# Performance work log

Hardware: AMD Instinct MI355X
Metric: run time of the kernel (lower is better)

Reference implementation:

```python
import jax, jax.numpy as jnp
import numpy as np
import math

DIM = 768
HEADS = 12
HEAD_DIM = DIM // HEADS
LENS_T = 64
LENS_S = 256
NTOK = LENS_T + LENS_S
BATCH = 32
MLP_HIDDEN = 4 * DIM
KEEP_RATIO = 0.7
LENS_KEEP = math.ceil(KEEP_RATIO * LENS_S)  # 180, static
NEG_INF = -1e9  # finite stand-in for masked_fill(-inf); mask is all-False here
LN_EPS = 1e-5


def layer_norm(x, g, b):
    m = jnp.mean(x, axis=-1, keepdims=True)
    v = jnp.var(x, axis=-1, keepdims=True)
    return (x - m) * jax.lax.rsqrt(v + LN_EPS) * g + b


def attention(x_normed, w_qkv, w_proj, b_proj, mask):
    # x_normed: [B,N,C]; torch: qkv Linear (no bias), split heads, softmax(qk*scale), proj
    B, N, C = x_normed.shape
    qkv = (x_normed @ w_qkv.T).reshape(B, N, 3, HEADS, HEAD_DIM)
    qkv = jnp.transpose(qkv, (2, 0, 3, 1, 4))  # [3,B,H,N,Dh]
    q, k, v = qkv[0], qkv[1], qkv[2]
    scores = jnp.einsum('bhqd,bhkd->bhqk', q, k) * (HEAD_DIM ** -0.5)
    scores = jnp.where(mask[:, None, None, :], NEG_INF, scores)
    attn = jax.nn.softmax(scores, axis=-1)  # [B,H,N,N]
    out = jnp.einsum('bhqk,bhkd->bhqd', attn, v)
    out = jnp.transpose(out, (0, 2, 1, 3)).reshape(B, N, C)
    return out @ w_proj.T + b_proj, attn


def mlp(x, w_fc1, b_fc1, w_fc2, b_fc2):
    h = jax.nn.gelu(x @ w_fc1.T + b_fc1, approximate=False)
    return h @ w_fc2.T + b_fc2


def candidate_topk(attn_all, tmpl_mask_f):
    # attn_all: [B,H,N,N]; template->search block, masked mean over template rows,
    # mean over heads, sort descending, split into keep/removed.
    attn_ts = attn_all[:, :, :LENS_T, LENS_T:]  # [B,H,T,S]
    w = tmpl_mask_f[:, None, :, None]  # [B,1,T,1]
    denom = jnp.sum(tmpl_mask_f, axis=1)[:, None, None]  # [B,1,1]
    scores = jnp.sum(attn_ts * w, axis=2) / denom  # [B,H,S] mean over kept template rows
    scores = jnp.mean(scores, axis=1)  # [B,S] mean over heads
    order = jnp.argsort(-scores, axis=1)  # descending
    return order[:, :LENS_KEEP], order[:, LENS_KEEP:]


def gather_tokens(tokens, topk_idx):
    tokens_t = tokens[:, :LENS_T]
    tokens_s = tokens[:, LENS_T:]
    kept = jnp.take_along_axis(tokens_s, topk_idx[:, :, None], axis=1)
    return jnp.concatenate([tokens_t, kept], axis=1)


def setup_inputs() -> dict:
    key = jax.random.key(0)
    ks = jax.random.split(key, 12)
    s = 0.02
    return {
        'x_rgb': jax.random.normal(ks[0], (BATCH, NTOK, DIM), jnp.float32),
        'x_tir': jax.random.normal(ks[1], (BATCH, NTOK, DIM), jnp.float32),
        'global_index_t': jax.random.randint(ks[2], (BATCH, LENS_T), 0, 64).astype(jnp.int64),
        'global_index_s': jax.random.randint(ks[3], (BATCH, LENS_S), 0, 256).astype(jnp.int64),
        'mask': jnp.zeros((BATCH, NTOK), dtype=bool),
        'cte_template_mask': jnp.ones((BATCH, LENS_T), dtype=bool),
        'keep_ratio_search': 0,
        'js_loss': jax.random.normal(ks[4], (1,), jnp.float32),
        'g1': jnp.ones((DIM,), jnp.float32),
        'b1': jnp.zeros((DIM,), jnp.float32),
        'w_qkv': jax.random.normal(ks[5], (3 * DIM, DIM), jnp.float32) * s,
        'w_proj': jax.random.normal(ks[6], (DIM, DIM), jnp.float32) * s,
        'b_proj': jnp.zeros((DIM,), jnp.float32),
        'g2': jnp.ones((DIM,), jnp.float32),
        'b2': jnp.zeros((DIM,), jnp.float32),
        'w_fc1': jax.random.normal(ks[7], (MLP_HIDDEN, DIM), jnp.float32) * s,
        'b_fc1': jnp.zeros((MLP_HIDDEN,), jnp.float32),
        'w_fc2': jax.random.normal(ks[8], (DIM, MLP_HIDDEN), jnp.float32) * s,
        'b_fc2': jnp.zeros((DIM,), jnp.float32),
    }


def reference(x_rgb, x_tir, global_index_t, global_index_s, mask, cte_template_mask,
              keep_ratio_search, js_loss, g1, b1, w_qkv, w_proj, b_proj, g2, b2,
              w_fc1, b_fc1, w_fc2, b_fc2):
    # dual-stream shared-weight attention
    rgb_attn_out, corrmap_rgb = attention(layer_norm(x_rgb, g1, b1), w_qkv, w_proj, b_proj, mask)
    tir_attn_out, corrmap_tir = attention(layer_norm(x_tir, g1, b1), w_qkv, w_proj, b_proj, mask)
    x_rgb = x_rgb + rgb_attn_out  # drop_path = Identity
    x_tir = x_tir + tir_attn_out

    # candidate elimination: both streams use the SAME fused attention map,
    # so the topk is identical for rgb and tir (torch calls it twice, same result)
    attn_all = corrmap_rgb + corrmap_tir
    tmpl_mask_f = cte_template_mask.astype(attn_all.dtype)
    topk_idx, non_topk_idx = candidate_topk(attn_all, tmpl_mask_f)
    x_rgb = gather_tokens(x_rgb, topk_idx)
    x_tir = gather_tokens(x_tir, topk_idx)
    global_index_s_new = jnp.take_along_axis(global_index_s, topk_idx, axis=1)
    removed_index_s = jnp.take_along_axis(global_index_s, non_topk_idx, axis=1)

    x_rgb = x_rgb + mlp(layer_norm(x_rgb, g2, b2), w_fc1, b_fc1, w_fc2, b_fc2)
    x_tir = x_tir + mlp(layer_norm(x_tir, g2, b2), w_fc1, b_fc1, w_fc2, b_fc2)
    return (x_rgb, x_tir, global_index_t, global_index_s_new, removed_index_s,
            corrmap_rgb, corrmap_tir, js_loss)
```

## Files before the change

### kernel.cpp

```cpp
#include <hip/hip_runtime.h>

typedef long long LL;
typedef unsigned short ushort_t;
typedef __attribute__((ext_vector_type(8))) short bfrag;
typedef __attribute__((ext_vector_type(8))) _Float16 hfrag;
typedef __attribute__((ext_vector_type(4))) float facc;
typedef __attribute__((ext_vector_type(4))) unsigned short us4;

constexpr int CDIM  = 768;
constexpr int HEADS = 12;
constexpr int LT    = 64;
constexpr int NTOK  = 320;
constexpr int BATCH = 32;
constexpr int LKEEP = 180;
constexpr int LREM  = 76;
constexpr int NK    = 244;

constexpr LL O_XRGB = 0;
constexpr LL O_XTIR = 5996544;
constexpr LL O_GIT  = 11993088;
constexpr LL O_GSN  = 11995136;
constexpr LL O_REM  = 12000896;
constexpr LL O_CR   = 12003328;
constexpr LL O_CT   = 51324928;
constexpr LL O_JS   = 90646528;

constexpr LL W_X1   = 0;
constexpr LL W_X1G  = 15728640;
constexpr LL W_XN   = 27746304;
constexpr LL W_QKV  = 35610624;
constexpr LL W_ATT  = 59596800;

constexpr LL SZH = 7864320;

__device__ inline ushort_t cvt_bf16(float f) {
    union { float f; unsigned u; } x; x.f = f;
    unsigned u = x.u + 0x7fffu + ((x.u >> 16) & 1u);
    return (ushort_t)(u >> 16);
}
union h16u { _Float16 h; ushort_t u; };

#define GLL(gp, lp) __builtin_amdgcn_global_load_lds( \
    (const __attribute__((address_space(1))) unsigned int*)(gp), \
    (__attribute__((address_space(3))) unsigned int*)(lp), 16, 0, 0)

__device__ inline void xcd_decode(int& bx, int& by) {
    int gx = gridDim.x;
    int nwg = gx * gridDim.y;
    int bid = blockIdx.y * gx + blockIdx.x;
    int q = nwg >> 3, r = nwg & 7;
    int xcd = bid & 7, i = bid >> 3;
    int wg = (xcd < r ? xcd * (q + 1) : r * (q + 1) + (xcd - r) * q) + i;
    bx = wg % gx;
    by = wg / gx;
}

__global__ __launch_bounds__(256)
void prep_weights(const float* __restrict__ wproj, const float* __restrict__ wqkv,
                  const float* __restrict__ wfc1, const float* __restrict__ wfc2,
                  ushort_t* __restrict__ WPROJb, ushort_t* __restrict__ Wh,
                  ushort_t* __restrict__ Wl, ushort_t* __restrict__ WFC1b,
                  ushort_t* __restrict__ WFC2b)
{
    int i = blockIdx.x * 256 + threadIdx.x;
    if (i < 147456) {
        int j = i * 4;
        float4 v = *(const float4*)(wproj + j);
        us4 o;
        o[0] = cvt_bf16(v.x); o[1] = cvt_bf16(v.y);
        o[2] = cvt_bf16(v.z); o[3] = cvt_bf16(v.w);
        *(us4*)(WPROJb + j) = o;
    } else if (i < 589824) {
        int j = (i - 147456) * 4;
        float4 v = *(const float4*)(wqkv + j);
        us4 h, l;
        #pragma unroll
        for (int k = 0; k < 4; ++k) {
            float f = (k == 0 ? v.x : k == 1 ? v.y : k == 2 ? v.z : v.w);
            h16u hh, ll;
            hh.h = (_Float16)f;
            ll.h = (_Float16)(f - (float)hh.h);
            h[k] = hh.u; l[k] = ll.u;
        }
        *(us4*)(Wh + j) = h;
        *(us4*)(Wl + j) = l;
    } else if (i < 1179648) {
        int j = (i - 589824) * 4;
        float4 v = *(const float4*)(wfc1 + j);
        us4 o;
        o[0] = cvt_bf16(v.x); o[1] = cvt_bf16(v.y);
        o[2] = cvt_bf16(v.z); o[3] = cvt_bf16(v.w);
        *(us4*)(WFC1b + j) = o;
    } else {
        int j = (i - 1179648) * 4;
        float4 v = *(const float4*)(wfc2 + j);
        us4 o;
        o[0] = cvt_bf16(v.x); o[1] = cvt_bf16(v.y);
        o[2] = cvt_bf16(v.z); o[3] = cvt_bf16(v.w);
        *(us4*)(WFC2b + j) = o;
    }
}

template<bool B16OUT>
__global__ __launch_bounds__(256)
void ln_kernel(const float* __restrict__ x, const float* __restrict__ g,
               const float* __restrict__ bta, void* __restrict__ y)
{
    LL row = blockIdx.x;
    const float* xr = x + row * 768;
    int t = threadIdx.x;
    float v0 = xr[t], v1 = xr[t + 256], v2 = xr[t + 512];
    __shared__ float red[256];
    red[t] = v0 + v1 + v2;
    __syncthreads();
    for (int s = 128; s; s >>= 1) { if (t < s) red[t] += red[t + s]; __syncthreads(); }
    float mean = red[0] / 768.0f;
    __syncthreads();
    float d0 = v0 - mean, d1 = v1 - mean, d2 = v2 - mean;
    red[t] = d0 * d0 + d1 * d1 + d2 * d2;
    __syncthreads();
    for (int s = 128; s; s >>= 1) { if (t < s) red[t] += red[t + s]; __syncthreads(); }
    float var = red[0] / 768.0f;
    float rs = 1.0f / sqrtf(var + 1e-5f);
    float o0 = d0 * rs * g[t]       + bta[t];
    float o1 = d1 * rs * g[t + 256] + bta[t + 256];
    float o2 = d2 * rs * g[t + 512] + bta[t + 512];
    if (B16OUT) {
        ushort_t* yr = (ushort_t*)y + row * 768;
        yr[t] = cvt_bf16(o0); yr[t + 256] = cvt_bf16(o1); yr[t + 512] = cvt_bf16(o2);
    } else {
        float* yr = (float*)y + row * 768;
        yr[t] = o0; yr[t + 256] = o1; yr[t + 512] = o2;
    }
}

__global__ __launch_bounds__(256)
void ln_f16x2(const float* __restrict__ x0, const float* __restrict__ x1,
              const float* __restrict__ g, const float* __restrict__ bta,
              ushort_t* __restrict__ ybase)
{
    int row = blockIdx.x;
    int mod = row >= 10240;
    int lrow = row - mod * 10240;
    const float* xr = (mod ? x1 : x0) + (LL)lrow * 768;
    ushort_t* yh = ybase + (LL)mod * 2 * SZH + (LL)lrow * 768;
    ushort_t* yl = yh + SZH;
    int t = threadIdx.x;
    float v0 = xr[t], v1 = xr[t + 256], v2 = xr[t + 512];
    __shared__ float red[256];
    red[t] = v0 + v1 + v2;
    __syncthreads();
    for (int s = 128; s; s >>= 1) { if (t < s) red[t] += red[t + s]; __syncthreads(); }
    float mean = red[0] / 768.0f;
    __syncthreads();
    float d0 = v0 - mean, d1 = v1 - mean, d2 = v2 - mean;
    red[t] = d0 * d0 + d1 * d1 + d2 * d2;
    __syncthreads();
    for (int s = 128; s; s >>= 1) { if (t < s) red[t] += red[t + s]; __syncthreads(); }
    float var = red[0] / 768.0f;
    float rs = 1.0f / sqrtf(var + 1e-5f);
    #pragma unroll
    for (int c = 0; c < 3; ++c) {
        float d = (c == 0 ? d0 : c == 1 ? d1 : d2);
        int idx = t + c * 256;
        float o = d * rs * g[idx] + bta[idx];
        h16u hi, lo;
        hi.h = (_Float16)o;
        lo.h = (_Float16)(o - (float)hi.h);
        yh[idx] = hi.u;
        yl[idx] = lo.u;
    }
}

__global__ __launch_bounds__(256)
void gemm_qkv(const ushort_t* __restrict__ Ah, const ushort_t* __restrict__ Al,
              const ushort_t* __restrict__ Bh, const ushort_t* __restrict__ Bl,
              ushort_t* __restrict__ Q1, ushort_t* __restrict__ Q2,
              ushort_t* __restrict__ K1, ushort_t* __restrict__ K2,
              ushort_t* __restrict__ Vt)
{
    __shared__ ushort_t Ahs[8192], Als[8192], Bhs[8192], Bls[8192];
    int bx, by;
    xcd_decode(bx, by);
    const int t = threadIdx.x;
    const int wave = t >> 6, lane = t & 63;
    const int wr = wave >> 1, wc = wave & 1;
    const int lr = lane & 15, lh = lane >> 4;
    const LL bm = (LL)by * 128, bn = (LL)bx * 128;
    const bool vt = (bx >= 12);

    facc acc[4][4];
    #pragma unroll
    for (int i = 0; i < 4; ++i)
        #pragma unroll
        for (int j = 0; j < 4; ++j) acc[i][j] = (facc)(0.0f);

    const LL soff = (bm + wave * 16 + (lane >> 2)) * (LL)768 + (lane & 3) * 8;
    const LL boff = (bn + wave * 16 + (lane >> 2)) * (LL)768 + (lane & 3) * 8;
    const LL a64 = (LL)64 * 768;

    GLL(Ah + soff,       &Ahs[wave * 512]);
    GLL(Ah + soff + a64, &Ahs[2048 + wave * 512]);
    GLL(Bh + boff,       &Bhs[wave * 512]);
    GLL(Bh + boff + a64, &Bhs[2048 + wave * 512]);
    if (!vt) {
        GLL(Al + soff,       &Als[wave * 512]);
        GLL(Al + soff + a64, &Als[2048 + wave * 512]);
        GLL(Bl + boff,       &Bls[wave * 512]);
        GLL(Bl + boff + a64, &Bls[2048 + wave * 512]);
    }
    __syncthreads();

    int cur = 0;
    for (int k0 = 0; k0 < 768; k0 += 32) {
        int nb = (cur ^ 1) * 4096;
        if (k0 + 32 < 768) {
            GLL(Ah + soff + k0 + 32,       &Ahs[nb + wave * 512]);
            GLL(Ah + soff + k0 + 32 + a64, &Ahs[nb + 2048 + wave * 512]);
            GLL(Bh + boff + k0 + 32,       &Bhs[nb + wave * 512]);
            GLL(Bh + boff + k0 + 32 + a64, &Bhs[nb + 2048 + wave * 512]);
            if (!vt) {
                GLL(Al + soff + k0 + 32,       &Als[nb + wave * 512]);
                GLL(Al + soff + k0 + 32 + a64, &Als[nb + 2048 + wave * 512]);
                GLL(Bl + boff + k0 + 32,       &Bls[nb + wave * 512]);
                GLL(Bl + boff + k0 + 32 + a64, &Bls[nb + 2048 + wave * 512]);
            }
        }
        int cb = cur * 4096;
        hfrag ah[4], bh[4];
        #pragma unroll
        for (int mi = 0; mi < 4; ++mi)
            ah[mi] = *(const hfrag*)&Ahs[cb + (wr * 64 + mi * 16 + lr) * 32 + lh * 8];
        #pragma unroll
        for (int ni = 0; ni < 4; ++ni)
            bh[ni] = *(const hfrag*)&Bhs[cb + (wc * 64 + ni * 16 + lr) * 32 + lh * 8];
        if (!vt) {
            hfrag al[4], bl[4];
            #pragma unroll
            for (int mi = 0; mi < 4; ++mi)
                al[mi] = *(const hfrag*)&Als[cb + (wr * 64 + mi * 16 + lr) * 32 + lh * 8];
            #pragma unroll
            for (int ni = 0; ni < 4; ++ni)
                bl[ni] = *(const hfrag*)&Bls[cb + (wc * 64 + ni * 16 + lr) * 32 + lh * 8];
            #pragma unroll
            for (int mi = 0; mi < 4; ++mi)
                #pragma unroll
                for (int ni = 0; ni < 4; ++ni) {
                    acc[mi][ni] = __builtin_amdgcn_mfma_f32_16x16x32_f16(al[mi], bh[ni], acc[mi][ni], 0, 0, 0);
                    acc[mi][ni] = __builtin_amdgcn_mfma_f32_16x16x32_f16(ah[mi], bl[ni], acc[mi][ni], 0, 0, 0);
                    acc[mi][ni] = __builtin_amdgcn_mfma_f32_16x16x32_f16(ah[mi], bh[ni], acc[mi][ni], 0, 0, 0);
                }
        } else {
            #pragma unroll
            for (int mi = 0; mi < 4; ++mi)
                #pragma unroll
                for (int ni = 0; ni < 4; ++ni)
                    acc[mi][ni] = __builtin_amdgcn_mfma_f32_16x16x32_f16(ah[mi], bh[ni], acc[mi][ni], 0, 0, 0);
        }
        __syncthreads();
        cur ^= 1;
    }

    #pragma unroll
    for (int mi = 0; mi < 4; ++mi)
        #pragma unroll
        for (int ni = 0; ni < 4; ++ni)
            #pragma unroll
            for (int j = 0; j < 4; ++j) {
                int r = (int)bm + wr * 64 + mi * 16 + lh * 4 + j;
                int c = (int)bn + wc * 64 + ni * 16 + lr;
                int b = r / 320, tt = r - b * 320;
                int s = c / 768, rem = c - s * 768;
                int h = rem >> 6, d = rem & 63;
                LL hb = (LL)(b * 12 + h) * 20480;
                float v = acc[mi][ni][j];
                if (s == 2) {
                    Vt[hb + d * 320 + tt] = cvt_bf16(v);
                } else {
                    h16u a1, a2;
                    a1.h = (_Float16)v;
                    a2.h = (_Float16)(v - (float)a1.h);
                    LL idx = hb + (LL)tt * 64 + d;
                    if (s == 0) { Q1[idx] = a1.u; Q2[idx] = a2.u; }
                    else        { K1[idx] = a1.u; K2[idx] = a2.u; }
                }
            }
}

__global__ __launch_bounds__(256, 2)
void fused_attn(const ushort_t* __restrict__ Qh, const ushort_t* __restrict__ Qm,
                const ushort_t* __restrict__ Kh, const ushort_t* __restrict__ Km,
                const ushort_t* __restrict__ Vt,
                float* __restrict__ corr, ushort_t* __restrict__ attb,
                double* __restrict__ part, int mod)
{
    __shared__ __align__(128) unsigned char lds[81920];
    constexpr int PS = 40960;

    const int t = threadIdx.x;
    const int wave = t >> 6, lane = t & 63;
    const int lr = lane & 15, lh = lane >> 4;
    const int id  = blockIdx.x;
    const int xcd = id & 7;
    const int rem = id >> 3;
    const int grp = rem / 5;
    const int r0i = rem - grp * 5;
    const int bh  = grp * 8 + xcd;
    const int b = bh / 12, h = bh - b * 12;
    const int r0 = r0i * 64;
    const LL kvbase = (LL)bh * 20480;

    const LL qoff = kvbase + (LL)(r0 + wave * 16 + lr) * 64 + lh * 8;
    hfrag qh0 = *(const hfrag*)(Qh + qoff), qh1 = *(const hfrag*)(Qh + qoff + 32);
    hfrag qm0 = *(const hfrag*)(Qm + qoff), qm1 = *(const hfrag*)(Qm + qoff + 32);

    facc sacc[20];
    #pragma unroll
    for (int ct = 0; ct < 20; ++ct) sacc[ct] = (facc)(0.0f);

    #pragma unroll
    for (int ha = 0; ha < 5; ++ha) {
        if (ha) __syncthreads();
        #pragma unroll
        for (int i = 0; i < 4; ++i) {
            int id2 = wave * 4 + i;
            int s = id2 >> 3, c = id2 & 7;
            int local = c * 1024 + lane * 16;
            int row = local >> 7;
            int sb = local ^ ((row & 7) << 4);
            LL src = kvbase + (LL)ha * 4096 + (sb >> 1);
            const ushort_t* kp = (s == 0) ? Kh : Km;
            GLL(kp + src, &lds[s * 8192 + c * 1024]);
        }
        __syncthreads();

        #pragma unroll
        for (int ctl = 0; ctl < 4; ++ctl) {
            int tokl = ctl * 16 + lr;
            int x = (tokl & 7) << 4;
            const unsigned char* kb = lds + tokl * 128;
            int o0 = (lh * 16) ^ x;
            int o1 = (64 + lh * 16) ^ x;
            hfrag kh0 = *(const hfrag*)(kb + o0);
            hfrag kh1 = *(const hfrag*)(kb + o1);
            hfrag km0 = *(const hfrag*)(kb + 8192 + o0);
            hfrag km1 = *(const hfrag*)(kb + 8192 + o1);
            facc a = sacc[ha * 4 + ctl];
            a = __builtin_amdgcn_mfma_f32_16x16x32_f16(qm0, kh0, a, 0, 0, 0);
            a = __builtin_amdgcn_mfma_f32_16x16x32_f16(qh0, km0, a, 0, 0, 0);
            a = __builtin_amdgcn_mfma_f32_16x16x32_f16(qh0, kh0, a, 0, 0, 0);
            a = __builtin_amdgcn_mfma_f32_16x16x32_f16(qm1, kh1, a, 0, 0, 0);
            a = __builtin_amdgcn_mfma_f32_16x16x32_f16(qh1, km1, a, 0, 0, 0);
            a = __builtin_amdgcn_mfma_f32_16x16x32_f16(qh1, kh1, a, 0, 0, 0);
            sacc[ha * 4 + ctl] = a;
        }
    }

    __syncthreads();

    #pragma unroll
    for (int i = 0; i < 10; ++i) {
        int chunk = wave * 10 + i;
        int gs = chunk * 1024 + lane * 16;
        int d = gs / 640;
        int w = gs - d * 640;
        int sb = d * 640 + (w ^ ((d & 7) << 4));
        GLL(Vt + kvbase + (sb >> 1), &lds[chunk * 1024]);
    }

    float rs4[4];
    #pragma unroll
    for (int j = 0; j < 4; ++j) {
        float m = sacc[0][j];
        #pragma unroll
        for (int ct = 1; ct < 20; ++ct) m = fmaxf(m, sacc[ct][j]);
        #pragma unroll
        for (int o = 1; o < 16; o <<= 1) m = fmaxf(m, __shfl_xor(m, o, 64));
        m *= 0.125f;
        float s = 0.0f;
        #pragma unroll
        for (int ct = 0; ct < 20; ++ct) {
            float e = expf(sacc[ct][j] * 0.125f - m);
            sacc[ct][j] = e;
            s += e;
        }
        #pragma unroll
        for (int o = 1; o < 16; o <<= 1) s += __shfl_xor(s, o, 64);
        float rs = 1.0f / s;
        rs4[j] = rs;

        int prow = wave * 16 + lh * 4 + j;
        int xr = (prow & 7) << 4;
        #pragma unroll
        for (int ct = 0; ct < 20; ++ct) {
            int pcol = ct * 16 + lr;
            *(ushort_t*)(lds + PS + prow * 640 + ((pcol * 2) ^ xr)) =
                cvt_bf16(sacc[ct][j] * rs);
        }
    }

    __syncthreads();

    facc oacc[4];
    #pragma unroll
    for (int dt = 0; dt < 4; ++dt) oacc[dt] = (facc)(0.0f);
    int prow2 = wave * 16 + lr;
    int xp = (prow2 & 7) << 4;
    #pragma unroll
    for (int k0 = 0; k0 < 10; ++k0) {
        bfrag pa = *(const bfrag*)(lds + PS + prow2 * 640 + ((k0 * 64 + lh * 16) ^ xp));
        #pragma unroll
        for (int dt = 0; dt < 4; ++dt) {
            int dcol = dt * 16 + lr;
            bfrag vb = *(const bfrag*)(lds + dcol * 640 + ((k0 * 64 + lh * 16) ^ ((dcol & 7) << 4)));
            oacc[dt] = __builtin_amdgcn_mfma_f32_16x16x32_bf16(pa, vb, oacc[dt], 0, 0, 0);
        }
    }
    #pragma unroll
    for (int dt = 0; dt < 4; ++dt)
        #pragma unroll
        for (int j = 0; j < 4; ++j) {
            int grow = r0 + wave * 16 + lh * 4 + j;
            int gcol = h * 64 + dt * 16 + lr;
            attb[(LL)(b * 320 + grow) * 768 + gcol] = cvt_bf16(oacc[dt][j]);
        }

    __syncthreads();

    #pragma unroll
    for (int ct = 0; ct < 20; ++ct) {
        int pcol = ct * 16 + lr;
        #pragma unroll
        for (int j = 0; j < 4; ++j) {
            int prow = wave * 16 + lh * 4 + j;
            *(float*)(lds + (prow * 320 + pcol) * 4) = sacc[ct][j] * rs4[j];
        }
    }
    __syncthreads();

    float* crow = corr + (LL)bh * 102400 + (LL)r0 * 320;
    #pragma unroll
    for (int i = 0; i < 20; ++i) {
        int idx = i * 256 + t;
        int row = idx / 80, c4 = idx - row * 80;
        float4 v = *(const float4*)(lds + (row * 320 + c4 * 4) * 4);
        *(float4*)(crow + row * 320 + c4 * 4) = v;
    }

    if (r0i == 0) {
        double s64 = 0.0;
        for (int r = 0; r < 64; ++r)
            s64 += (double)*(const float*)(lds + (r * 320 + 64 + t) * 4);
        part[((LL)mod * 384 + bh) * 256 + t] = s64;
    }
}

template<int EPI>
__global__ __launch_bounds__(256)
void gemm_mfma(const ushort_t* __restrict__ A, const ushort_t* __restrict__ B,
               void* __restrict__ Cv, const float* __restrict__ bias,
               const float* __restrict__ res, const int* __restrict__ amap,
               int K, int lda, int ldb, int ldc, int ldres)
{
    __shared__ ushort_t As[8192];
    __shared__ ushort_t Bs[8192];
    int bx, by;
    xcd_decode(bx, by);
    const int t = threadIdx.x;
    const int wave = t >> 6, lane = t & 63;
    const int wr = wave >> 1, wc = wave & 1;
    const LL bm = (LL)by * 128, bn = (LL)bx * 128;

    facc acc[4][4];
    #pragma unroll
    for (int i = 0; i < 4; ++i)
        #pragma unroll
        for (int j = 0; j < 4; ++j) acc[i][j] = (facc)(0.0f);

    const int lr = lane & 15, lh = lane >> 4;
    int r1 = (int)bm + wave * 16 + (lane >> 2);
    int r2 = r1 + 64;
    if (amap) { r1 = amap[r1]; r2 = amap[r2]; }
    const ushort_t* gA1 = A + (LL)r1 * lda + (lane & 3) * 8;
    const ushort_t* gA2 = A + (LL)r2 * lda + (lane & 3) * 8;
    const ushort_t* gB = B + (bn + wave * 16 + (lane >> 2)) * ldb + (lane & 3) * 8;
    const LL b64 = (LL)64 * ldb;

    GLL(gA1,       &As[wave * 512]);
    GLL(gA2,       &As[2048 + wave * 512]);
    GLL(gB,        &Bs[wave * 512]);
    GLL(gB + b64,  &Bs[2048 + wave * 512]);
    __syncthreads();

    int cur = 0;
    for (int k0 = 0; k0 < K; k0 += 32) {
        int nb = (cur ^ 1) * 4096;
        if (k0 + 32 < K) {
            GLL(gA1 + k0 + 32,       &As[nb + wave * 512]);
            GLL(gA2 + k0 + 32,       &As[nb + 2048 + wave * 512]);
            GLL(gB + k0 + 32,        &Bs[nb + wave * 512]);
            GLL(gB + k0 + 32 + b64,  &Bs[nb + 2048 + wave * 512]);
        }
        int cb = cur * 4096;
        bfrag a[4], b[4];
        #pragma unroll
        for (int m = 0; m < 4; ++m)
            a[m] = *(const bfrag*)&As[cb + (wr * 64 + m * 16 + lr) * 32 + lh * 8];
        #pragma unroll
        for (int n = 0; n < 4; ++n)
            b[n] = *(const bfrag*)&Bs[cb + (wc * 64 + n * 16 + lr) * 32 + lh * 8];
        #pragma unroll
        for (int m = 0; m < 4; ++m)
            #pragma unroll
            for (int n = 0; n < 4; ++n)
                acc[m][n] = __builtin_amdgcn_mfma_f32_16x16x32_bf16(a[m], b[n], acc[m][n], 0, 0, 0);
        __syncthreads();
        cur ^= 1;
    }

    #pragma unroll
    for (int m = 0; m < 4; ++m) {
        #pragma unroll
        for (int n = 0; n < 4; ++n) {
            #pragma unroll
            for (int j = 0; j < 4; ++j) {
                LL r = bm + wr * 64 + m * 16 + lh * 4 + j;
                LL c = bn + wc * 64 + n * 16 + lr;
                float v = acc[m][n][j] + bias[c];
                if (EPI == 1) {
                    v = 0.5f * v * (erff(v * 0.70710678118654752f) + 1.0f);
                    ((ushort_t*)Cv)[r * ldc + c] = cvt_bf16(v);
                } else {
                    LL rr = amap ? (LL)amap[r] : r;
                    v += res[rr * ldres + c];
                    ((float*)Cv)[r * ldc + c] = v;
                }
            }
        }
    }
}

__global__ __launch_bounds__(256)
void rank_all(const double* __restrict__ part, const int* __restrict__ gis,
              const int* __restrict__ git, const float* __restrict__ js,
              int* __restrict__ srcmap, float* __restrict__ out)
{
    int b = blockIdx.x, j = threadIdx.x;
    double acc = 0.0;
    for (int h = 0; h < 12; ++h) {
        LL i0 = ((LL)(b * 12 + h)) * 256 + j;
        acc += (part[i0] + part[98304 + i0]) / 64.0;
    }
    double sj = acc / 12.0;
    __shared__ double s[256];
    __shared__ int sord[256];
    s[j] = sj;
    __syncthreads();
    int r = 0;
    for (int i = 0; i < 256; ++i) {
        double si = s[i];
        r += (si > sj) || (si == sj && i < j);
    }
    sord[r] = j;
    float gv = (float)gis[b * 256 + j];
    if (r < LKEEP) out[O_GSN + b * LKEEP + r] = gv;
    else           out[O_REM + b * LREM + (r - LKEEP)] = gv;
    __syncthreads();
    if (j < NK) {
        int src = (j < LT) ? j : (LT + sord[j - LT]);
        srcmap[b * NK + j] = b * NTOK + src;
    }
    if (j < 64) out[O_GIT + b * 64 + j] = (float)git[b * 64 + j];
    if (b == 0 && j == 0) out[O_JS] = js[0];
}

extern "C" void kernel_launch(void* const* d_in, const int* in_sizes, int n_in,
                              void* d_out, int out_size, void* d_ws, size_t ws_size,
                              hipStream_t stream)
{
    const float* xin_m[2] = { (const float*)d_in[0], (const float*)d_in[1] };
    const int*   git    = (const int*)d_in[2];
    const int*   gis    = (const int*)d_in[3];
    const float* js     = (const float*)d_in[7];
    const float* g1     = (const float*)d_in[8];
    const float* b1     = (const float*)d_in[9];
    const float* w_qkv  = (const float*)d_in[10];
    const float* w_proj = (const float*)d_in[11];
    const float* b_proj = (const float*)d_in[12];
    const float* g2     = (const float*)d_in[13];
    const float* b2     = (const float*)d_in[14];
    const float* w_fc1  = (const float*)d_in[15];
    const float* b_fc1  = (const float*)d_in[16];
    const float* w_fc2  = (const float*)d_in[17];
    const float* b_fc2  = (const float*)d_in[18];

    float* out = (float*)d_out;
    float* ws  = (float*)d_ws;

    ushort_t* Xbase = (ushort_t*)(ws + W_X1);
    float*    X1c  = ws + W_X1;
    ushort_t* ATTb0 = (ushort_t*)(ws + W_XN);
    ushort_t* ATTb1 = ATTb0 + SZH;
    ushort_t* QK  = (ushort_t*)(ws + W_QKV);
    ushort_t* Qh2 = QK,           *Qm2 = QK + SZH;
    ushort_t* Kh2 = QK + 2 * SZH, *Km2 = QK + 3 * SZH;
    ushort_t* Wh  = (ushort_t*)(ws + W_ATT);
    ushort_t* Wl  = Wh + 1769472;
    ushort_t* Vt  = (ushort_t*)(ws + W_ATT + 2000000);
    double*   part = (double*)(ws + W_ATT + 6000000);
    int*      srcmap = (int*)(ws + W_ATT + 6400000);
    ushort_t* WPROJb = (ushort_t*)(ws + W_X1G);
    ushort_t* WFC1b  = (ushort_t*)(ws + W_X1G + 294912);
    ushort_t* WFC2b  = (ushort_t*)(ws + W_X1G + 1474560);
    ushort_t* XN2b   = (ushort_t*)(ws + W_XN);
    ushort_t* H1b    = (ushort_t*)(ws + W_QKV);

    prep_weights<<<dim3(6912), dim3(256), 0, stream>>>(
        w_proj, w_qkv, w_fc1, w_fc2, WPROJb, Wh, Wl, WFC1b, WFC2b);

    ln_f16x2<<<dim3(2 * BATCH * NTOK), dim3(256), 0, stream>>>(
        xin_m[0], xin_m[1], g1, b1, Xbase);

    for (int m = 0; m < 2; ++m) {
        float* corr = out + (m ? O_CT : O_CR);
        ushort_t* ATTbm = m ? ATTb1 : ATTb0;
        ushort_t* Xh = Xbase + (LL)m * 2 * SZH;
        ushort_t* Xl = Xh + SZH;

        gemm_qkv<<<dim3(18, 80), dim3(256), 0, stream>>>(
            Xh, Xl, Wh, Wl, Qh2, Qm2, Kh2, Km2, Vt);

        fused_attn<<<dim3(1920), dim3(256), 0, stream>>>(
            Qh2, Qm2, Kh2, Km2, Vt, corr, ATTbm, part, m);
    }

    rank_all<<<dim3(BATCH), dim3(256), 0, stream>>>(part, gis, git, js, srcmap, out);

    for (int m = 0; m < 2; ++m) {
        gemm_mfma<2><<<dim3(6, 61), dim3(256), 0, stream>>>(
            m ? ATTb1 : ATTb0, WPROJb, X1c + (LL)m * 5996544, b_proj,
            xin_m[m], srcmap, 768, 768, 768, 768, 768);
    }

    ln_kernel<true><<<dim3(2 * BATCH * NK), dim3(256), 0, stream>>>(
        X1c, g2, b2, XN2b);

    gemm_mfma<1><<<dim3(24, 122), dim3(256), 0, stream>>>(
        XN2b, WFC1b, H1b, b_fc1, nullptr, nullptr, 768, 768, 768, 3072, 0);

    gemm_mfma<2><<<dim3(6, 122), dim3(256), 0, stream>>>(
        H1b, WFC2b, out + O_XRGB, b_fc2, X1c, nullptr, 3072, 3072, 3072, 768, 768);
}
```

Baseline: 932.8 us.

## Add 256x256-tile 512-thread GEMM with 4-stage LDS pipeline for FC1

Replaces the generic 128-tile FC1 GEMM (GELU epilogue) with a dedicated kernel that uses 256x256 output tiles, 8 waves, and a 4-deep ring of direct global-to-LDS loads with explicit vmcnt waits and setprio around MFMA bursts. Larger tiles raise arithmetic intensity and cut global traffic. The deeper pipeline hides load latency. The cost is one block per CU, 128KB of LDS, heavy register use, and fewer blocks (732), which may hurt wave occupancy and tail balance. M=15616 rows are covered exactly by 61 tiles, and the kernel relies on a swizzled layout and on xcd_decode.

```diff
diff --git a/kernel.cpp b/kernel.cpp
--- a/kernel.cpp
+++ b/kernel.cpp
@@ -540,6 +540,106 @@
     }
 }
 
+__global__ __launch_bounds__(512, 1)
+void gemm256_fc1(const ushort_t* __restrict__ A, const ushort_t* __restrict__ B,
+                 ushort_t* __restrict__ C, const float* __restrict__ bias)
+{
+    __shared__ ushort_t As[32768];
+    __shared__ ushort_t Bs[32768];
+    int bx, by;
+    xcd_decode(bx, by);
+    const int tid = threadIdx.x;
+    const int wid = tid >> 6, lane = tid & 63;
+    const int wr = wid >> 2, wc = wid & 3;
+    const int lr = lane & 15, lh = lane >> 4;
+    const LL bm = (LL)by * 256, bn = (LL)bx * 256;
+
+    facc acc[8][4];
+    #pragma unroll
+    for (int m = 0; m < 8; ++m)
+        #pragma unroll
+        for (int n = 0; n < 4; ++n) acc[m][n] = (facc)(0.0f);
+
+    int srow[2], sk[2];
+    #pragma unroll
+    for (int l = 0; l < 2; ++l) {
+        int o = l * 8192 + tid * 16;
+        int rg = o >> 10;
+        int o10 = o & 1023;
+        int op = o10 ^ (((o10 >> 9) & 1) << 5);
+        srow[l] = rg * 16 + (op >> 6);
+        sk[l]   = (op & 63) >> 1;
+    }
+
+    #define STAGE256(kt) { \
+        int _bo = ((kt) & 3) * 8192; \
+        _Pragma("unroll") \
+        for (int l = 0; l < 2; ++l) { \
+            GLL(A + (bm + srow[l]) * (LL)768 + (kt) * 32 + sk[l], \
+                &As[_bo + l * 4096 + tid * 8]); \
+            GLL(B + (bn + srow[l]) * (LL)768 + (kt) * 32 + sk[l], \
+                &Bs[_bo + l * 4096 + tid * 8]); \
+        } }
+
+    STAGE256(0); STAGE256(1); STAGE256(2);
+    asm volatile("s_waitcnt vmcnt(8)" ::: "memory");
+    __builtin_amdgcn_sched_barrier(0);
+    __builtin_amdgcn_s_barrier();
+
+    const int b10 = lr * 64 + lh * 16;
+    const int sb = (b10 ^ (((lr >> 3) & 1) << 5)) >> 1;
+
+    for (int kt = 0; kt < 24; ++kt) {
+        int cb = (kt & 3) * 8192;
+        bfrag a[4], b[4];
+        #pragma unroll
+        for (int m = 0; m < 4; ++m)
+            a[m] = *(const bfrag*)&As[cb + ((wr * 8 + m) << 9) + sb];
+        #pragma unroll
+        for (int n = 0; n < 4; ++n)
+            b[n] = *(const bfrag*)&Bs[cb + ((wc * 4 + n) << 9) + sb];
+        if (kt + 3 < 24) STAGE256(kt + 3);
+        __builtin_amdgcn_s_setprio(1);
+        #pragma unroll
+        for (int m = 0; m < 4; ++m)
+            #pragma unroll
+            for (int n = 0; n < 4; ++n)
+                acc[m][n] = __builtin_amdgcn_mfma_f32_16x16x32_bf16(a[m], b[n], acc[m][n], 0, 0, 0);
+        __builtin_amdgcn_s_setprio(0);
+        #pragma unroll
+        for (int m = 0; m < 4; ++m)
+            a[m] = *(const bfrag*)&As[cb + ((wr * 8 + 4 + m) << 9) + sb];
+        __builtin_amdgcn_s_setprio(1);
+        #pragma unroll
+        for (int m = 0; m < 4; ++m)
+            #pragma unroll
+            for (int n = 0; n < 4; ++n)
+                acc[4 + m][n] = __builtin_amdgcn_mfma_f32_16x16x32_bf16(a[m], b[n], acc[4 + m][n], 0, 0, 0);
+        __builtin_amdgcn_s_setprio(0);
+        if (kt < 23) {
+            if (kt < 21)      asm volatile("s_waitcnt vmcnt(8)" ::: "memory");
+            else if (kt == 21) asm volatile("s_waitcnt vmcnt(4)" ::: "memory");
+            else               asm volatile("s_waitcnt vmcnt(0)" ::: "memory");
+            __builtin_amdgcn_sched_barrier(0);
+            __builtin_amdgcn_s_barrier();
+        }
+    }
+    #undef STAGE256
+
+    #pragma unroll
+    for (int m = 0; m < 8; ++m)
+        #pragma unroll
+        for (int n = 0; n < 4; ++n)
+            #pragma unroll
+            for (int j = 0; j < 4; ++j) {
+                LL r = bm + wr * 128 + m * 16 + lh * 4 + j;
+                LL c = bn + wc * 64 + n * 16 + lr;
+                float v = acc[m][n][j] + bias[c];
+                v = 0.5f * v * (erff(v * 0.70710678118654752f) + 1.0f);
+                C[r * 3072 + c] = cvt_bf16(v);
+            }
+}
+
 __global__ __launch_bounds__(256)
 void rank_all(const double* __restrict__ part, const int* __restrict__ gis,
               const int* __restrict__ git, const float* __restrict__ js,
@@ -645,8 +745,7 @@
     ln_kernel<true><<<dim3(2 * BATCH * NK), dim3(256), 0, stream>>>(
         X1c, g2, b2, XN2b);
 
-    gemm_mfma<1><<<dim3(24, 122), dim3(256), 0, stream>>>(
-        XN2b, WFC1b, H1b, b_fc1, nullptr, nullptr, 768, 768, 768, 3072, 0);
+    gemm256_fc1<<<dim3(12, 61), dim3(512), 0, stream>>>(XN2b, WFC1b, H1b, b_fc1);
 
     gemm_mfma<2><<<dim3(6, 122), dim3(256), 0, stream>>>(
         H1b, WFC2b, out + O_XRGB, b_fc2, X1c, nullptr, 3072, 3072, 3072, 768, 768);
```

Result: slower. 982.4 us (+5.3%).
